# Kernel tuning notes

Hardware: AMD Instinct MI355X
Metric: run time of the kernel (lower is better)

Reference implementation:

```python
import jax, jax.numpy as jnp
import numpy as np

D_MODEL, D_STATE, D_CONV, EXPAND = 1024, 16, 4, 2
D_INNER = EXPAND * D_MODEL
BATCH, SEQ = 2, 2048


def setup_inputs() -> dict:
    key = jax.random.key(0)
    ks = jax.random.split(key, 10)
    s = lambda fan_in: 1.0 / np.sqrt(fan_in)
    return {
        "x": jax.random.normal(ks[0], (BATCH, SEQ, D_MODEL), jnp.float32),
        "W_in": jax.random.normal(ks[1], (2 * D_INNER, D_MODEL), jnp.float32) * s(D_MODEL),
        "w_conv": jax.random.normal(ks[2], (D_INNER, D_CONV), jnp.float32) * s(D_CONV),
        "b_conv": jax.random.normal(ks[3], (D_INNER,), jnp.float32) * 0.02,
        "W_x": jax.random.normal(ks[4], (D_INNER + 2 * D_STATE, D_INNER), jnp.float32) * s(D_INNER),
        "W_dt": jax.random.normal(ks[5], (D_INNER, D_INNER), jnp.float32) * s(D_INNER),
        "b_dt": jax.random.normal(ks[6], (D_INNER,), jnp.float32) * 0.02,
        "A_log": jnp.log(jax.random.uniform(ks[7], (D_INNER, D_STATE), jnp.float32, 1e-4, 1.0)),
        "D": jnp.ones((D_INNER,), jnp.float32),
        "W_out": jax.random.normal(ks[8], (D_MODEL, D_INNER), jnp.float32) * s(D_INNER),
    }


def _depthwise_causal_conv(x, w, b):
    # x: (B, L, C), w: (C, K), causal (left-pad K-1), matches conv1d(padding=K-1)[..., :L]
    K = w.shape[1]
    L = x.shape[1]
    xp = jnp.pad(x, ((0, 0), (K - 1, 0), (0, 0)))
    out = b
    for k in range(K):  # K is tiny (4)
        out = out + xp[:, k:k + L, :] * w[:, k]
    return out


def _selective_scan(x, delta, Bm, Cm, A, Dv):
    # x, delta: (B, L, d_inner); Bm, Cm: (B, L, d_state)
    def step(state, inp):
        x_t, d_t, B_t, C_t = inp  # (B,d_inner),(B,d_inner),(B,d_state),(B,d_state)
        decay = jnp.exp(d_t[..., None] * A)          # (B, d_inner, d_state)
        state = decay * state + B_t[:, None, :] * x_t[..., None]
        y_t = jnp.einsum('bds,bs->bd', state, C_t) + x_t * Dv
        return state, y_t

    init = jnp.zeros((x.shape[0], x.shape[2], A.shape[1]), x.dtype)
    xs = tuple(jnp.swapaxes(a, 0, 1) for a in (x, delta, Bm, Cm))
    _, ys = jax.lax.scan(step, init, xs)             # ys: (L, B, d_inner)
    return jnp.swapaxes(ys, 0, 1)


def reference(x, W_in, w_conv, b_conv, W_x, W_dt, b_dt, A_log, D, W_out):
    silu = jax.nn.silu
    xz = x @ W_in.T                                   # (B, L, 2*d_inner)
    x_inner, z = jnp.split(xz, 2, axis=-1)
    x_conv = silu(_depthwise_causal_conv(x_inner, w_conv, b_conv))
    x_dbl = x_conv @ W_x.T                            # (B, L, d_inner + 2*d_state)
    delta, Bm, Cm = jnp.split(x_dbl, [D_INNER, D_INNER + D_STATE], axis=-1)
    delta = jax.nn.softplus(delta @ W_dt.T + b_dt)
    A = -jnp.exp(A_log.astype(jnp.float32))
    y = _selective_scan(x_conv, delta, Bm, Cm, A, D)
    y = y * silu(z)
    return y @ W_out.T
```

## Files before the change

kernel.cpp:

```cpp
#include <hip/hip_runtime.h>
#include <hip/hip_bf16.h>


#define BATCH 2
#define SEQ   2048
#define DM    1024
#define DI    2048
#define DS    16
#define T_TOK (BATCH * SEQ)

#define CL 64
#define NC 32

typedef __bf16 v8bf __attribute__((ext_vector_type(8)));
typedef float  v4f  __attribute__((ext_vector_type(4)));

__device__ __forceinline__ void gld16(const void* g, void* l) {
    __builtin_amdgcn_global_load_lds(
        (const __attribute__((address_space(1))) void*)g,
        (__attribute__((address_space(3))) void*)l, 16, 0, 0);
}

__device__ __forceinline__ float b2f(__hip_bfloat16 v) { return __bfloat162float(v); }

__global__ void detect_dtype(const unsigned* __restrict__ Dptr, int* __restrict__ flag) {
    if (threadIdx.x == 0 && blockIdx.x == 0)
        *flag = (Dptr[0] == 0x3F803F80u) ? 1 : 0;
}

__device__ __forceinline__ float load_in(const void* p, size_t i, int isbf) {
    return isbf ? b2f(((const __hip_bfloat16*)p)[i]) : ((const float*)p)[i];
}

#define NBIG0 (T_TOK * DM)
#define NBIG1 (4096 * DM)
#define NBIG2 (DI * DI)
#define NBIG3 (DM * DI)
__global__ void convert_big(const void* __restrict__ s0, const void* __restrict__ s1,
                            const void* __restrict__ s2, const void* __restrict__ s3,
                            __hip_bfloat16* __restrict__ d0, __hip_bfloat16* __restrict__ d1,
                            __hip_bfloat16* __restrict__ d2, __hip_bfloat16* __restrict__ d3,
                            const int* __restrict__ flag) {
    if (*flag) return;
    size_t e = ((size_t)blockIdx.x * 256 + threadIdx.x) * 8;
    const float* src; __hip_bfloat16* dst;
    if (e < NBIG0)                      { src = (const float*)s0 + e;                 dst = d0 + e; }
    else if (e < NBIG0 + NBIG1)         { e -= NBIG0; src = (const float*)s1 + e;     dst = d1 + e; }
    else if (e < NBIG0 + NBIG1 + NBIG2) { e -= NBIG0 + NBIG1; src = (const float*)s2 + e; dst = d2 + e; }
    else                                { e -= NBIG0 + NBIG1 + NBIG2; src = (const float*)s3 + e; dst = d3 + e; }
    const float4 a = *(const float4*)src;
    const float4 b = *(const float4*)(src + 4);
    __bf16 o[8] = {(__bf16)a.x,(__bf16)a.y,(__bf16)a.z,(__bf16)a.w,
                   (__bf16)b.x,(__bf16)b.y,(__bf16)b.z,(__bf16)b.w};
    *(uint4*)dst = *(uint4*)&o[0];
}

__global__ void convert_small(const void* __restrict__ wconv, const void* __restrict__ bconv,
                              const void* __restrict__ bdt, const void* __restrict__ dv,
                              __hip_bfloat16* __restrict__ wconvb, __hip_bfloat16* __restrict__ bconvb,
                              __hip_bfloat16* __restrict__ bdtb, __hip_bfloat16* __restrict__ db,
                              const int* __restrict__ flag) {
    const int isbf = *flag;
    const int i = blockIdx.x * 256 + threadIdx.x;
    if (i < 8192)        wconvb[i]        = __float2bfloat16(load_in(wconv, i, isbf));
    else if (i < 10240)  bconvb[i - 8192] = __float2bfloat16(load_in(bconv, i - 8192, isbf));
    else if (i < 12288)  bdtb[i - 10240]  = __float2bfloat16(load_in(bdt, i - 10240, isbf));
    else if (i < 14336)  db[i - 12288]    = __float2bfloat16(load_in(dv, i - 12288, isbf));
}

template <int MODE, int TN>
__global__ __launch_bounds__(256) void gemm_bt(
    const __hip_bfloat16* __restrict__ Ac, const void* __restrict__ Araw,
    const __hip_bfloat16* __restrict__ Bc, const void* __restrict__ Braw,
    void* __restrict__ out0, void* __restrict__ out1,
    const __hip_bfloat16* __restrict__ bias,
    const int* __restrict__ flag,
    int M, int N, int K)
{
    constexpr int NF = TN / 32;
    constexpr int ASLOT = 512;
    constexpr int BSLOT = TN * 4;
    __shared__ v8bf Asv[2 * ASLOT];
    __shared__ v8bf Bsv[2 * BSLOT];

    const int isbf = *flag;
    const __hip_bfloat16* A  = (isbf && Araw) ? (const __hip_bfloat16*)Araw : Ac;
    const __hip_bfloat16* Bw = (isbf && Braw) ? (const __hip_bfloat16*)Braw : Bc;

    const int nx = gridDim.x;
    const int nblk = nx * gridDim.y;
    const int id = blockIdx.y * nx + blockIdx.x;
    const int sid = (id & 7) * (nblk >> 3) + (id >> 3);
    const int bxs = sid % nx;
    const int bys = sid / nx;

    const int tid  = threadIdx.x;
    const int bm   = bys * 128;
    const int bn   = bxs * TN;
    const int w    = tid >> 6;
    const int lane = tid & 63;
    const int wm   = (w >> 1) * 64;
    const int wn   = (w & 1) * (TN / 2);
    const int lrow  = lane & 15;
    const int lquad = lane >> 4;

    v4f acc[4][NF];
#pragma unroll
    for (int i = 0; i < 4; i++)
#pragma unroll
        for (int j = 0; j < NF; j++) acc[i][j] = (v4f){0.f, 0.f, 0.f, 0.f};

    const int r0 = tid >> 2;
    const int q0 = (tid & 3) ^ ((r0 >> 1) & 3);
    const __hip_bfloat16* gA0 = A  + (size_t)(bm + r0) * K + q0 * 8;
    const __hip_bfloat16* gA1 = A  + (size_t)(bm + 64 + r0) * K + q0 * 8;
    const __hip_bfloat16* gB0 = Bw + (size_t)(bn + r0) * K + q0 * 8;
    const __hip_bfloat16* gB1 = Bw + (size_t)(bn + 64 + r0) * K + q0 * 8;
    char* lA0 = (char*)Asv + tid * 16;
    char* lA1 = (char*)Asv + 4096 + tid * 16;
    char* lB0 = (char*)Bsv + tid * 16;
    char* lB1 = (char*)Bsv + 4096 + tid * 16;

    const int swz = lquad ^ ((lrow >> 1) & 3);
    int sA[4], sB[NF];
#pragma unroll
    for (int i = 0; i < 4; i++) sA[i] = (wm + i * 16 + lrow) * 4 + swz;
#pragma unroll
    for (int i = 0; i < NF; i++) sB[i] = (wn + i * 16 + lrow) * 4 + swz;

    const int NIT = K >> 5;
    gld16(gA0, lA0);
    gld16(gA1, lA1);
    gld16(gB0, lB0);
    if (TN == 128) gld16(gB1, lB1);

    int k = 32;
    for (int it = 0; it < NIT; ++it) {
        const int cb = it & 1;
        __syncthreads();
        if (it + 1 < NIT) {
            const int pa = (cb ^ 1) * 8192;
            const int pb = (cb ^ 1) * (BSLOT * 16);
            gld16(gA0 + k, lA0 + pa);
            gld16(gA1 + k, lA1 + pa);
            gld16(gB0 + k, lB0 + pb);
            if (TN == 128) gld16(gB1 + k, lB1 + pb);
            k += 32;
        }
        const int ca = cb * ASLOT;
        const int cbb = cb * BSLOT;
        v8bf af[4], bfr[NF];
#pragma unroll
        for (int i = 0; i < 4; i++)
            af[i] = Asv[ca + sA[i]];
#pragma unroll
        for (int i = 0; i < NF; i++)
            bfr[i] = Bsv[cbb + sB[i]];
#pragma unroll
        for (int mi = 0; mi < 4; mi++)
#pragma unroll
            for (int ni = 0; ni < NF; ni++)
                acc[mi][ni] = __builtin_amdgcn_mfma_f32_16x16x32_bf16(
                    af[mi], bfr[ni], acc[mi][ni], 0, 0, 0);
    }

#pragma unroll
    for (int mi = 0; mi < 4; mi++) {
#pragma unroll
        for (int ni = 0; ni < NF; ni++) {
#pragma unroll
            for (int r = 0; r < 4; r++) {
                const int grow = bm + wm + mi * 16 + lquad * 4 + r;
                const int gcol = bn + wn + ni * 16 + lrow;
                const float v = acc[mi][ni][r];
                if (MODE == 0) {
                    ((__hip_bfloat16*)out0)[(size_t)grow * N + gcol] = __float2bfloat16(v);
                } else if (MODE == 1) {
                    if (gcol < 2048) {
                        ((__hip_bfloat16*)out0)[(size_t)grow * 2048 + gcol] = __float2bfloat16(v);
                    } else if (gcol < 2080) {
                        ((float*)out1)[(size_t)grow * 32 + (gcol - 2048)] = v;
                    }
                } else if (MODE == 2) {
                    const float x = v + b2f(bias[gcol]);
                    const float sp = (x > 15.f) ? x : __logf(1.f + __expf(x));
                    ((__hip_bfloat16*)out0)[(size_t)grow * 2048 + gcol] = __float2bfloat16(sp);
                } else {
                    if (isbf)
                        ((__hip_bfloat16*)out0)[(size_t)grow * N + gcol] = __float2bfloat16(v);
                    else
                        ((float*)out0)[(size_t)grow * N + gcol] = v;
                }
            }
        }
    }
}

__global__ void prep_A(const void* __restrict__ A_log, float* __restrict__ Amat,
                       const int* __restrict__ flag) {
    const int isbf = *flag;
    const int i = blockIdx.x * 256 + threadIdx.x;
    if (i < DI * DS) Amat[i] = -__expf(load_in(A_log, i, isbf));
}

__global__ void pad_Wx(const void* __restrict__ Wx, __hip_bfloat16* __restrict__ Wxp,
                       const int* __restrict__ flag) {
    const int isbf = *flag;
    const size_t e = ((size_t)blockIdx.x * 256 + threadIdx.x) * 8;
    if (e >= (size_t)2176 * 2048) return;
    if (e >= (size_t)2080 * 2048) {
        __bf16 z[8] = {};
        *(uint4*)(Wxp + e) = *(uint4*)&z[0];
        return;
    }
    if (isbf) {
        *(uint4*)(Wxp + e) = *(const uint4*)((const __hip_bfloat16*)Wx + e);
    } else {
        const float* src = (const float*)Wx + e;
        const float4 a = *(const float4*)src;
        const float4 b = *(const float4*)(src + 4);
        __bf16 o[8] = {(__bf16)a.x,(__bf16)a.y,(__bf16)a.z,(__bf16)a.w,
                       (__bf16)b.x,(__bf16)b.y,(__bf16)b.z,(__bf16)b.w};
        *(uint4*)(Wxp + e) = *(uint4*)&o[0];
    }
}

__global__ __launch_bounds__(256) void conv_silu(
    const __hip_bfloat16* __restrict__ xz,
    const __hip_bfloat16* __restrict__ wconv,
    const __hip_bfloat16* __restrict__ bconv,
    __hip_bfloat16* __restrict__ xconv)
{
    const int idx = blockIdx.x * 256 + threadIdx.x;
    const int c8 = (idx & 255) << 3;
    const int tg = idx >> 8;
    const int tl = tg & (SEQ - 1);

    __bf16 wl[32], bl[8];
    *(uint4*)&wl[0]  = *(const uint4*)(wconv + c8 * 4);
    *(uint4*)&wl[8]  = *(const uint4*)(wconv + c8 * 4 + 8);
    *(uint4*)&wl[16] = *(const uint4*)(wconv + c8 * 4 + 16);
    *(uint4*)&wl[24] = *(const uint4*)(wconv + c8 * 4 + 24);
    *(uint4*)&bl[0]  = *(const uint4*)(bconv + c8);

    float acc[8];
#pragma unroll
    for (int cc = 0; cc < 8; cc++) acc[cc] = (float)bl[cc];

#pragma unroll
    for (int k = 0; k < 4; k++) {
        const int ts = tl - 3 + k;
        if (ts >= 0) {
            __bf16 xl[8];
            *(uint4*)&xl[0] = *(const uint4*)(xz + (size_t)(tg - 3 + k) * 4096 + c8);
#pragma unroll
            for (int cc = 0; cc < 8; cc++)
                acc[cc] += (float)wl[cc * 4 + k] * (float)xl[cc];
        }
    }

    __bf16 o[8];
#pragma unroll
    for (int cc = 0; cc < 8; cc++) {
        const float s = acc[cc] / (1.f + __expf(-acc[cc]));
        o[cc] = (__bf16)s;
    }
    *(uint4*)(xconv + (size_t)tg * DI + c8) = *(uint4*)&o[0];
}

__global__ __launch_bounds__(256) void scan_p1(
    const __hip_bfloat16* __restrict__ delta, const __hip_bfloat16* __restrict__ xconv,
    const float* __restrict__ BC, const float* __restrict__ Amat,
    float* __restrict__ Pws, float* __restrict__ Sws)
{
    const int d = blockIdx.x * 256 + threadIdx.x;
    const int c = blockIdx.y;
    const int b = blockIdx.z;
    const int tg0 = b * SEQ + c * CL;

    __shared__ float bc[CL * 32];
    for (int i = threadIdx.x; i < CL * 32; i += 256) bc[i] = BC[(size_t)tg0 * 32 + i];
    __syncthreads();

    float Areg[DS];
#pragma unroll
    for (int s = 0; s < DS; s++) Areg[s] = Amat[d * DS + s];

    float P[DS], S[DS];
#pragma unroll
    for (int s = 0; s < DS; s++) { P[s] = 1.f; S[s] = 0.f; }

    for (int i = 0; i < CL; i++) {
        const size_t tg = tg0 + i;
        const float dl = b2f(delta[tg * DI + d]);
        const float x  = b2f(xconv[tg * DI + d]);
#pragma unroll
        for (int s = 0; s < DS; s++) {
            const float e = __expf(dl * Areg[s]);
            P[s] *= e;
            S[s] = e * S[s] + bc[i * 32 + s] * x;
        }
    }

    const size_t base = (((size_t)b * NC + c) * DI + d) * DS;
#pragma unroll
    for (int s = 0; s < DS; s += 4) {
        *(float4*)(Pws + base + s) = make_float4(P[s], P[s+1], P[s+2], P[s+3]);
        *(float4*)(Sws + base + s) = make_float4(S[s], S[s+1], S[s+2], S[s+3]);
    }
}

__global__ void scan_p2(float* __restrict__ Pws, float* __restrict__ Sws) {
    const int idx = blockIdx.x * 256 + threadIdx.x;
    const int b  = idx >> 15;
    const int ds = idx & 32767;
    float carry = 0.f;
    for (int c = 0; c < NC; c++) {
        const size_t a = (((size_t)b * NC + c) << 15) + ds;
        const float p  = Pws[a];
        const float sv = Sws[a];
        Sws[a] = carry;
        carry = p * carry + sv;
    }
}

__global__ __launch_bounds__(256) void scan_p3(
    const __hip_bfloat16* __restrict__ delta, const __hip_bfloat16* __restrict__ xconv,
    const float* __restrict__ BC, const float* __restrict__ Amat,
    const float* __restrict__ Sws, const __hip_bfloat16* __restrict__ xz,
    const __hip_bfloat16* __restrict__ Dv, __hip_bfloat16* __restrict__ yg)
{
    const int d = blockIdx.x * 256 + threadIdx.x;
    const int c = blockIdx.y;
    const int b = blockIdx.z;
    const int tg0 = b * SEQ + c * CL;

    __shared__ float bc[CL * 32];
    for (int i = threadIdx.x; i < CL * 32; i += 256) bc[i] = BC[(size_t)tg0 * 32 + i];
    __syncthreads();

    float Areg[DS];
#pragma unroll
    for (int s = 0; s < DS; s++) Areg[s] = Amat[d * DS + s];

    const size_t base = (((size_t)b * NC + c) * DI + d) * DS;
    float S[DS];
#pragma unroll
    for (int s = 0; s < DS; s += 4) {
        const float4 v = *(const float4*)(Sws + base + s);
        S[s] = v.x; S[s+1] = v.y; S[s+2] = v.z; S[s+3] = v.w;
    }
    const float Dd = b2f(Dv[d]);

    for (int i = 0; i < CL; i++) {
        const size_t tg = tg0 + i;
        const float dl = b2f(delta[tg * DI + d]);
        const float x  = b2f(xconv[tg * DI + d]);
        float y = 0.f;
#pragma unroll
        for (int s = 0; s < DS; s++) {
            const float e = __expf(dl * Areg[s]);
            S[s] = e * S[s] + bc[i * 32 + s] * x;
            y += S[s] * bc[i * 32 + 16 + s];
        }
        y += x * Dd;
        const float z = b2f(xz[tg * 4096 + 2048 + d]);
        const float g = z / (1.f + __expf(-z));
        yg[tg * DI + d] = __float2bfloat16(y * g);
    }
}

extern "C" void kernel_launch(void* const* d_in, const int* in_sizes, int n_in,
                              void* d_out, int out_size, void* d_ws, size_t ws_size,
                              hipStream_t stream)
{
    const void* x_raw     = d_in[0];
    const void* W_in_raw  = d_in[1];
    const void* wconv_raw = d_in[2];
    const void* bconv_raw = d_in[3];
    const void* W_x_raw   = d_in[4];
    const void* W_dt_raw  = d_in[5];
    const void* b_dt_raw  = d_in[6];
    const void* A_log_raw = d_in[7];
    const void* D_raw     = d_in[8];
    const void* W_out_raw = d_in[9];

    char* ws = (char*)d_ws;
    size_t off = 0;
    auto alloc = [&](size_t bytes) { char* p = ws + off; off += (bytes + 255) & ~(size_t)255; return p; };
    int*            FLAG  = (int*)alloc(256);
    __hip_bfloat16* XB    = (__hip_bfloat16*)alloc((size_t)T_TOK * DM * 2);
    __hip_bfloat16* WINB  = (__hip_bfloat16*)alloc((size_t)4096 * DM * 2);
    __hip_bfloat16* WDTB  = (__hip_bfloat16*)alloc((size_t)DI * DI * 2);
    __hip_bfloat16* WOUTB = (__hip_bfloat16*)alloc((size_t)DM * DI * 2);
    __hip_bfloat16* WCONVB= (__hip_bfloat16*)alloc((size_t)DI * 4 * 2);
    __hip_bfloat16* BCONVB= (__hip_bfloat16*)alloc((size_t)DI * 2);
    __hip_bfloat16* BDTB  = (__hip_bfloat16*)alloc((size_t)DI * 2);
    __hip_bfloat16* DB    = (__hip_bfloat16*)alloc((size_t)DI * 2);
    __hip_bfloat16* XZ    = (__hip_bfloat16*)alloc((size_t)T_TOK * 4096 * 2);
    __hip_bfloat16* XCONV = (__hip_bfloat16*)alloc((size_t)T_TOK * DI * 2);
    __hip_bfloat16* DRAW  = (__hip_bfloat16*)alloc((size_t)T_TOK * DI * 2);
    __hip_bfloat16* WXPAD = (__hip_bfloat16*)alloc((size_t)2176 * DI * 2);
    float*          BC    = (float*)alloc((size_t)T_TOK * 32 * 4);
    __hip_bfloat16* DELTA = (__hip_bfloat16*)alloc((size_t)T_TOK * DI * 2);
    float*          AMAT  = (float*)alloc((size_t)DI * DS * 4);
    float*          PWS   = (float*)alloc((size_t)BATCH * NC * DI * DS * 4);
    float*          SWS   = (float*)alloc((size_t)BATCH * NC * DI * DS * 4);
    __hip_bfloat16* YG    = (__hip_bfloat16*)alloc((size_t)T_TOK * DI * 2);

    detect_dtype<<<1, 64, 0, stream>>>((const unsigned*)D_raw, FLAG);
    convert_big<<<(NBIG0 + NBIG1 + NBIG2 + NBIG3) / (256 * 8), 256, 0, stream>>>(
        x_raw, W_in_raw, W_dt_raw, W_out_raw, XB, WINB, WDTB, WOUTB, FLAG);
    convert_small<<<56, 256, 0, stream>>>(wconv_raw, bconv_raw, b_dt_raw, D_raw,
                                          WCONVB, BCONVB, BDTB, DB, FLAG);
    prep_A<<<(DI * DS + 255) / 256, 256, 0, stream>>>(A_log_raw, AMAT, FLAG);
    pad_Wx<<<(int)(((size_t)2176 * 2048 / 8 + 255) / 256), 256, 0, stream>>>(W_x_raw, WXPAD, FLAG);

    gemm_bt<0, 128><<<dim3(32, 32), 256, 0, stream>>>(
        XB, x_raw, WINB, W_in_raw, XZ, nullptr, nullptr, FLAG, T_TOK, 4096, DM);

    conv_silu<<<T_TOK, 256, 0, stream>>>(XZ, WCONVB, BCONVB, XCONV);

    gemm_bt<1, 128><<<dim3(17, 32), 256, 0, stream>>>(
        XCONV, nullptr, WXPAD, nullptr, DRAW, BC, nullptr, FLAG, T_TOK, 2176, DI);

    gemm_bt<2, 128><<<dim3(16, 32), 256, 0, stream>>>(
        DRAW, nullptr, WDTB, W_dt_raw, DELTA, nullptr, BDTB, FLAG, T_TOK, DI, DI);

    scan_p1<<<dim3(DI / 256, NC, BATCH), 256, 0, stream>>>(DELTA, XCONV, BC, AMAT, PWS, SWS);
    scan_p2<<<(BATCH * DI * DS) / 256, 256, 0, stream>>>(PWS, SWS);
    scan_p3<<<dim3(DI / 256, NC, BATCH), 256, 0, stream>>>(DELTA, XCONV, BC, AMAT, SWS, XZ, DB, YG);

    gemm_bt<3, 64><<<dim3(16, 32), 256, 0, stream>>>(
        YG, nullptr, WOUTB, W_out_raw, d_out, nullptr, nullptr, FLAG, T_TOK, DM, DI);
}
```

Baseline: 464.1 us.

## Add 256x256-tile 8-wave GEMM with 4-stage LDS pipeline for three projections

Adds a new bf16 MFMA GEMM kernel with 256x256 output tiles, 512 threads (8 waves), a 4-buffer global-to-LDS prefetch pipeline with explicit vmcnt waits, swizzled LDS layout, and block-id remapping across groups of eight. It replaces the older 128-wide-tile GEMM for the in-projection, x-projection and dt-projection. W_x padding grows from 2176 to 2304 rows so that N divides evenly by 256, which adds some wasted compute on zero rows. The aim is higher data reuse per tile and better overlap of loads with MFMA work. The cost is a large register footprint and fewer blocks per GPU.

```diff
diff --git a/kernel.cpp b/kernel.cpp
--- a/kernel.cpp
+++ b/kernel.cpp
@@ -66,6 +66,133 @@
     else if (i < 10240)  bconvb[i - 8192] = __float2bfloat16(load_in(bconv, i - 8192, isbf));
     else if (i < 12288)  bdtb[i - 10240]  = __float2bfloat16(load_in(bdt, i - 10240, isbf));
     else if (i < 14336)  db[i - 12288]    = __float2bfloat16(load_in(dv, i - 12288, isbf));
+}
+
+template <int MODE, int KDIM>
+__global__ __launch_bounds__(512, 2) void gemm8p(
+    const __hip_bfloat16* __restrict__ Ac, const void* __restrict__ Araw,
+    const __hip_bfloat16* __restrict__ Bc, const void* __restrict__ Braw,
+    void* __restrict__ out0, void* __restrict__ out1,
+    const __hip_bfloat16* __restrict__ bias,
+    const int* __restrict__ flag,
+    int N)
+{
+    constexpr int NT = KDIM >> 5;
+    __shared__ v8bf lds[8192];
+
+    const int isbf = *flag;
+    const __hip_bfloat16* A  = (isbf && Araw) ? (const __hip_bfloat16*)Araw : Ac;
+    const __hip_bfloat16* Bw = (isbf && Braw) ? (const __hip_bfloat16*)Braw : Bc;
+
+    const int nx = gridDim.x;
+    const int nblk = nx * gridDim.y;
+    const int id = blockIdx.y * nx + blockIdx.x;
+    const int sid = (id & 7) * (nblk >> 3) + (id >> 3);
+    const int bm = (sid / nx) * 256;
+    const int bn = (sid % nx) * 256;
+
+    const int tid   = threadIdx.x;
+    const int lane  = tid & 63;
+    const int w     = tid >> 6;
+    const int wr    = (w >> 2) * 128;
+    const int wc    = (w & 3) * 64;
+    const int lrow  = lane & 15;
+    const int lquad = lane >> 4;
+    const int swz   = lquad ^ ((lrow >> 1) & 3);
+
+    v4f acc[8][4];
+#pragma unroll
+    for (int i = 0; i < 8; i++)
+#pragma unroll
+        for (int j = 0; j < 4; j++) acc[i][j] = (v4f){0.f, 0.f, 0.f, 0.f};
+
+    const int r0 = tid >> 2;
+    const int q0 = (tid & 3) ^ ((r0 >> 1) & 3);
+    const __hip_bfloat16* gA0 = A  + (size_t)(bm + r0) * KDIM + q0 * 8;
+    const __hip_bfloat16* gA1 = gA0 + (size_t)128 * KDIM;
+    const __hip_bfloat16* gB0 = Bw + (size_t)(bn + r0) * KDIM + q0 * 8;
+    const __hip_bfloat16* gB1 = gB0 + (size_t)128 * KDIM;
+    char* lbase = (char*)&lds[0] + tid * 16;
+
+    int sA[8], sB[4];
+#pragma unroll
+    for (int i = 0; i < 8; i++) sA[i] = (wr + i * 16 + lrow) * 4 + swz;
+#pragma unroll
+    for (int i = 0; i < 4; i++) sB[i] = 1024 + (wc + i * 16 + lrow) * 4 + swz;
+
+#define STAGE8(kt, b) do {                         \
+        const size_t ko_ = (size_t)(kt) * 32;      \
+        char* d_ = lbase + (b) * 32768;            \
+        gld16(gA0 + ko_, d_);                      \
+        gld16(gA1 + ko_, d_ + 8192);               \
+        gld16(gB0 + ko_, d_ + 16384);              \
+        gld16(gB1 + ko_, d_ + 24576);              \
+    } while (0)
+
+    STAGE8(0, 0);
+    STAGE8(1, 1);
+    STAGE8(2, 2);
+
+#pragma unroll 4
+    for (int t = 0; t < NT; ++t) {
+        const int cb = t & 3;
+        if (t + 3 < NT) {
+            STAGE8(t + 3, (t + 3) & 3);
+            asm volatile("s_waitcnt vmcnt(12)" ::: "memory");
+        } else if (t + 3 == NT) {
+            asm volatile("s_waitcnt vmcnt(8)" ::: "memory");
+        } else if (t + 2 == NT) {
+            asm volatile("s_waitcnt vmcnt(4)" ::: "memory");
+        } else {
+            asm volatile("s_waitcnt vmcnt(0)" ::: "memory");
+        }
+        __builtin_amdgcn_s_barrier();
+
+        const v8bf* buf = &lds[0] + cb * 2048;
+        v8bf af[8], bfr[4];
+#pragma unroll
+        for (int i = 0; i < 8; i++) af[i] = buf[sA[i]];
+#pragma unroll
+        for (int i = 0; i < 4; i++) bfr[i] = buf[sB[i]];
+        asm volatile("s_waitcnt lgkmcnt(0)" ::: "memory");
+        __builtin_amdgcn_s_barrier();
+
+        __builtin_amdgcn_s_setprio(1);
+#pragma unroll
+        for (int mi = 0; mi < 8; mi++)
+#pragma unroll
+            for (int ni = 0; ni < 4; ni++)
+                acc[mi][ni] = __builtin_amdgcn_mfma_f32_16x16x32_bf16(
+                    af[mi], bfr[ni], acc[mi][ni], 0, 0, 0);
+        __builtin_amdgcn_s_setprio(0);
+    }
+#undef STAGE8
+
+#pragma unroll
+    for (int mi = 0; mi < 8; mi++) {
+#pragma unroll
+        for (int ni = 0; ni < 4; ni++) {
+#pragma unroll
+            for (int r = 0; r < 4; r++) {
+                const int grow = bm + wr + mi * 16 + lquad * 4 + r;
+                const int gcol = bn + wc + ni * 16 + lrow;
+                const float v = acc[mi][ni][r];
+                if (MODE == 0) {
+                    ((__hip_bfloat16*)out0)[(size_t)grow * N + gcol] = __float2bfloat16(v);
+                } else if (MODE == 1) {
+                    if (gcol < 2048) {
+                        ((__hip_bfloat16*)out0)[(size_t)grow * 2048 + gcol] = __float2bfloat16(v);
+                    } else if (gcol < 2080) {
+                        ((float*)out1)[(size_t)grow * 32 + (gcol - 2048)] = v;
+                    }
+                } else {
+                    const float x = v + b2f(bias[gcol]);
+                    const float sp = (x > 15.f) ? x : __logf(1.f + __expf(x));
+                    ((__hip_bfloat16*)out0)[(size_t)grow * 2048 + gcol] = __float2bfloat16(sp);
+                }
+            }
+        }
+    }
 }
 
 template <int MODE, int TN>
@@ -207,7 +334,7 @@
                        const int* __restrict__ flag) {
     const int isbf = *flag;
     const size_t e = ((size_t)blockIdx.x * 256 + threadIdx.x) * 8;
-    if (e >= (size_t)2176 * 2048) return;
+    if (e >= (size_t)2304 * 2048) return;
     if (e >= (size_t)2080 * 2048) {
         __bf16 z[8] = {};
         *(uint4*)(Wxp + e) = *(uint4*)&z[0];
@@ -400,7 +527,7 @@
     __hip_bfloat16* XZ    = (__hip_bfloat16*)alloc((size_t)T_TOK * 4096 * 2);
     __hip_bfloat16* XCONV = (__hip_bfloat16*)alloc((size_t)T_TOK * DI * 2);
     __hip_bfloat16* DRAW  = (__hip_bfloat16*)alloc((size_t)T_TOK * DI * 2);
-    __hip_bfloat16* WXPAD = (__hip_bfloat16*)alloc((size_t)2176 * DI * 2);
+    __hip_bfloat16* WXPAD = (__hip_bfloat16*)alloc((size_t)2304 * DI * 2);
     float*          BC    = (float*)alloc((size_t)T_TOK * 32 * 4);
     __hip_bfloat16* DELTA = (__hip_bfloat16*)alloc((size_t)T_TOK * DI * 2);
     float*          AMAT  = (float*)alloc((size_t)DI * DS * 4);
@@ -414,18 +541,18 @@
     convert_small<<<56, 256, 0, stream>>>(wconv_raw, bconv_raw, b_dt_raw, D_raw,
                                           WCONVB, BCONVB, BDTB, DB, FLAG);
     prep_A<<<(DI * DS + 255) / 256, 256, 0, stream>>>(A_log_raw, AMAT, FLAG);
-    pad_Wx<<<(int)(((size_t)2176 * 2048 / 8 + 255) / 256), 256, 0, stream>>>(W_x_raw, WXPAD, FLAG);
-
-    gemm_bt<0, 128><<<dim3(32, 32), 256, 0, stream>>>(
-        XB, x_raw, WINB, W_in_raw, XZ, nullptr, nullptr, FLAG, T_TOK, 4096, DM);
+    pad_Wx<<<(int)(((size_t)2304 * 2048 / 8 + 255) / 256), 256, 0, stream>>>(W_x_raw, WXPAD, FLAG);
+
+    gemm8p<0, 1024><<<dim3(16, 16), 512, 0, stream>>>(
+        XB, x_raw, WINB, W_in_raw, XZ, nullptr, nullptr, FLAG, 4096);
 
     conv_silu<<<T_TOK, 256, 0, stream>>>(XZ, WCONVB, BCONVB, XCONV);
 
-    gemm_bt<1, 128><<<dim3(17, 32), 256, 0, stream>>>(
-        XCONV, nullptr, WXPAD, nullptr, DRAW, BC, nullptr, FLAG, T_TOK, 2176, DI);
-
-    gemm_bt<2, 128><<<dim3(16, 32), 256, 0, stream>>>(
-        DRAW, nullptr, WDTB, W_dt_raw, DELTA, nullptr, BDTB, FLAG, T_TOK, DI, DI);
+    gemm8p<1, 2048><<<dim3(9, 16), 512, 0, stream>>>(
+        XCONV, nullptr, WXPAD, nullptr, DRAW, BC, nullptr, FLAG, 2304);
+
+    gemm8p<2, 2048><<<dim3(8, 16), 512, 0, stream>>>(
+        DRAW, nullptr, WDTB, W_dt_raw, DELTA, nullptr, BDTB, FLAG, 2048);
 
     scan_p1<<<dim3(DI / 256, NC, BATCH), 256, 0, stream>>>(DELTA, XCONV, BC, AMAT, PWS, SWS);
     scan_p2<<<(BATCH * DI * DS) / 256, 256, 0, stream>>>(PWS, SWS);
```

New measurement: 468.7 us. About the same (+1.0%).

## Fold W_dt into W_x weights to fuse delta projection GEMMs

Applied to the files above, without the earlier changes.

Precomputes the product of W_dt and the delta rows of W_x as a weight-only GEMM (after transposing W_x), so the per-token delta projection becomes a single GEMM with fused bias+softplus alongside the B/C outputs. This removes one token-sized GEMM and the intermediate DRAW buffer round trip. It also merges the A_log prep into convert_small. The cost is an extra transpose and a 2048^3 weight GEMM per call, and a change in rounding since the combined weight is rounded to bf16.

```diff
diff --git a/kernel.cpp b/kernel.cpp
--- a/kernel.cpp
+++ b/kernel.cpp
@@ -57,8 +57,10 @@
 
 __global__ void convert_small(const void* __restrict__ wconv, const void* __restrict__ bconv,
                               const void* __restrict__ bdt, const void* __restrict__ dv,
+                              const void* __restrict__ A_log,
                               __hip_bfloat16* __restrict__ wconvb, __hip_bfloat16* __restrict__ bconvb,
                               __hip_bfloat16* __restrict__ bdtb, __hip_bfloat16* __restrict__ db,
+                              float* __restrict__ Amat,
                               const int* __restrict__ flag) {
     const int isbf = *flag;
     const int i = blockIdx.x * 256 + threadIdx.x;
@@ -66,6 +68,68 @@
     else if (i < 10240)  bconvb[i - 8192] = __float2bfloat16(load_in(bconv, i - 8192, isbf));
     else if (i < 12288)  bdtb[i - 10240]  = __float2bfloat16(load_in(bdt, i - 10240, isbf));
     else if (i < 14336)  db[i - 12288]    = __float2bfloat16(load_in(dv, i - 12288, isbf));
+    else if (i < 47104)  Amat[i - 14336]  = -__expf(load_in(A_log, i - 14336, isbf));
+}
+
+__global__ __launch_bounds__(256) void transpose_wxd(
+    const void* __restrict__ Wx, __hip_bfloat16* __restrict__ WxdT,
+    const int* __restrict__ flag)
+{
+    const int isbf = *flag;
+    __shared__ __bf16 t[64][72];
+    const int bi = blockIdx.y * 64;
+    const int bj = blockIdx.x * 64;
+    const int rr = threadIdx.x >> 3;
+    const int c0 = (threadIdx.x & 7) * 8;
+
+#pragma unroll
+    for (int k = 0; k < 2; k++) {
+        const int r = rr + k * 32;
+        const size_t src = (size_t)(bi + r) * DI + bj + c0;
+        __bf16 o[8];
+        if (isbf) {
+            *(uint4*)&o[0] = *(const uint4*)((const __hip_bfloat16*)Wx + src);
+        } else {
+            const float* s = (const float*)Wx + src;
+            const float4 a = *(const float4*)s;
+            const float4 b = *(const float4*)(s + 4);
+            o[0]=(__bf16)a.x; o[1]=(__bf16)a.y; o[2]=(__bf16)a.z; o[3]=(__bf16)a.w;
+            o[4]=(__bf16)b.x; o[5]=(__bf16)b.y; o[6]=(__bf16)b.z; o[7]=(__bf16)b.w;
+        }
+        *(uint4*)&t[r][c0] = *(uint4*)&o[0];
+    }
+    __syncthreads();
+#pragma unroll
+    for (int k = 0; k < 2; k++) {
+        const int dr = rr + k * 32;
+        __bf16 o[8];
+#pragma unroll
+        for (int j = 0; j < 8; j++) o[j] = t[c0 + j][dr];
+        *(uint4*)(WxdT + (size_t)(bj + dr) * DI + bi + c0) = *(uint4*)&o[0];
+    }
+}
+
+__global__ void pad_bc(const void* __restrict__ Wx, __hip_bfloat16* __restrict__ Wxp,
+                       const int* __restrict__ flag) {
+    const int isbf = *flag;
+    const size_t e = ((size_t)blockIdx.x * 256 + threadIdx.x) * 8;
+    if (e >= (size_t)128 * DI) return;
+    const size_t base = (size_t)2048 * DI;
+    if (e >= (size_t)32 * DI) {
+        __bf16 z[8] = {};
+        *(uint4*)(Wxp + base + e) = *(uint4*)&z[0];
+        return;
+    }
+    if (isbf) {
+        *(uint4*)(Wxp + base + e) = *(const uint4*)((const __hip_bfloat16*)Wx + base + e);
+    } else {
+        const float* src = (const float*)Wx + base + e;
+        const float4 a = *(const float4*)src;
+        const float4 b = *(const float4*)(src + 4);
+        __bf16 o[8] = {(__bf16)a.x,(__bf16)a.y,(__bf16)a.z,(__bf16)a.w,
+                       (__bf16)b.x,(__bf16)b.y,(__bf16)b.z,(__bf16)b.w};
+        *(uint4*)(Wxp + base + e) = *(uint4*)&o[0];
+    }
 }
 
 template <int MODE, int TN>
@@ -175,16 +239,14 @@
                 const float v = acc[mi][ni][r];
                 if (MODE == 0) {
                     ((__hip_bfloat16*)out0)[(size_t)grow * N + gcol] = __float2bfloat16(v);
-                } else if (MODE == 1) {
+                } else if (MODE == 4) {
                     if (gcol < 2048) {
-                        ((__hip_bfloat16*)out0)[(size_t)grow * 2048 + gcol] = __float2bfloat16(v);
+                        const float x = v + b2f(bias[gcol]);
+                        const float sp = (x > 15.f) ? x : __logf(1.f + __expf(x));
+                        ((__hip_bfloat16*)out0)[(size_t)grow * 2048 + gcol] = __float2bfloat16(sp);
                     } else if (gcol < 2080) {
                         ((float*)out1)[(size_t)grow * 32 + (gcol - 2048)] = v;
                     }
-                } else if (MODE == 2) {
-                    const float x = v + b2f(bias[gcol]);
-                    const float sp = (x > 15.f) ? x : __logf(1.f + __expf(x));
-                    ((__hip_bfloat16*)out0)[(size_t)grow * 2048 + gcol] = __float2bfloat16(sp);
                 } else {
                     if (isbf)
                         ((__hip_bfloat16*)out0)[(size_t)grow * N + gcol] = __float2bfloat16(v);
@@ -193,35 +255,6 @@
                 }
             }
         }
-    }
-}
-
-__global__ void prep_A(const void* __restrict__ A_log, float* __restrict__ Amat,
-                       const int* __restrict__ flag) {
-    const int isbf = *flag;
-    const int i = blockIdx.x * 256 + threadIdx.x;
-    if (i < DI * DS) Amat[i] = -__expf(load_in(A_log, i, isbf));
-}
-
-__global__ void pad_Wx(const void* __restrict__ Wx, __hip_bfloat16* __restrict__ Wxp,
-                       const int* __restrict__ flag) {
-    const int isbf = *flag;
-    const size_t e = ((size_t)blockIdx.x * 256 + threadIdx.x) * 8;
-    if (e >= (size_t)2176 * 2048) return;
-    if (e >= (size_t)2080 * 2048) {
-        __bf16 z[8] = {};
-        *(uint4*)(Wxp + e) = *(uint4*)&z[0];
-        return;
-    }
-    if (isbf) {
-        *(uint4*)(Wxp + e) = *(const uint4*)((const __hip_bfloat16*)Wx + e);
-    } else {
-        const float* src = (const float*)Wx + e;
-        const float4 a = *(const float4*)src;
-        const float4 b = *(const float4*)(src + 4);
-        __bf16 o[8] = {(__bf16)a.x,(__bf16)a.y,(__bf16)a.z,(__bf16)a.w,
-                       (__bf16)b.x,(__bf16)b.y,(__bf16)b.z,(__bf16)b.w};
-        *(uint4*)(Wxp + e) = *(uint4*)&o[0];
     }
 }
 
@@ -399,7 +432,7 @@
     __hip_bfloat16* DB    = (__hip_bfloat16*)alloc((size_t)DI * 2);
     __hip_bfloat16* XZ    = (__hip_bfloat16*)alloc((size_t)T_TOK * 4096 * 2);
     __hip_bfloat16* XCONV = (__hip_bfloat16*)alloc((size_t)T_TOK * DI * 2);
-    __hip_bfloat16* DRAW  = (__hip_bfloat16*)alloc((size_t)T_TOK * DI * 2);
+    __hip_bfloat16* WXDT  = (__hip_bfloat16*)alloc((size_t)DI * DI * 2);
     __hip_bfloat16* WXPAD = (__hip_bfloat16*)alloc((size_t)2176 * DI * 2);
     float*          BC    = (float*)alloc((size_t)T_TOK * 32 * 4);
     __hip_bfloat16* DELTA = (__hip_bfloat16*)alloc((size_t)T_TOK * DI * 2);
@@ -411,21 +444,22 @@
     detect_dtype<<<1, 64, 0, stream>>>((const unsigned*)D_raw, FLAG);
     convert_big<<<(NBIG0 + NBIG1 + NBIG2 + NBIG3) / (256 * 8), 256, 0, stream>>>(
         x_raw, W_in_raw, W_dt_raw, W_out_raw, XB, WINB, WDTB, WOUTB, FLAG);
-    convert_small<<<56, 256, 0, stream>>>(wconv_raw, bconv_raw, b_dt_raw, D_raw,
-                                          WCONVB, BCONVB, BDTB, DB, FLAG);
-    prep_A<<<(DI * DS + 255) / 256, 256, 0, stream>>>(A_log_raw, AMAT, FLAG);
-    pad_Wx<<<(int)(((size_t)2176 * 2048 / 8 + 255) / 256), 256, 0, stream>>>(W_x_raw, WXPAD, FLAG);
+    convert_small<<<184, 256, 0, stream>>>(wconv_raw, bconv_raw, b_dt_raw, D_raw, A_log_raw,
+                                           WCONVB, BCONVB, BDTB, DB, AMAT, FLAG);
+    transpose_wxd<<<dim3(32, 32), 256, 0, stream>>>(W_x_raw, WXDT, FLAG);
+
+    gemm_bt<0, 128><<<dim3(16, 16), 256, 0, stream>>>(
+        WDTB, W_dt_raw, WXDT, nullptr, WXPAD, nullptr, nullptr, FLAG, DI, DI, DI);
+
+    pad_bc<<<128, 256, 0, stream>>>(W_x_raw, WXPAD, FLAG);
 
     gemm_bt<0, 128><<<dim3(32, 32), 256, 0, stream>>>(
         XB, x_raw, WINB, W_in_raw, XZ, nullptr, nullptr, FLAG, T_TOK, 4096, DM);
 
     conv_silu<<<T_TOK, 256, 0, stream>>>(XZ, WCONVB, BCONVB, XCONV);
 
-    gemm_bt<1, 128><<<dim3(17, 32), 256, 0, stream>>>(
-        XCONV, nullptr, WXPAD, nullptr, DRAW, BC, nullptr, FLAG, T_TOK, 2176, DI);
-
-    gemm_bt<2, 128><<<dim3(16, 32), 256, 0, stream>>>(
-        DRAW, nullptr, WDTB, W_dt_raw, DELTA, nullptr, BDTB, FLAG, T_TOK, DI, DI);
+    gemm_bt<4, 128><<<dim3(17, 32), 256, 0, stream>>>(
+        XCONV, nullptr, WXPAD, nullptr, DELTA, BC, BDTB, FLAG, T_TOK, 2176, DI);
 
     scan_p1<<<dim3(DI / 256, NC, BATCH), 256, 0, stream>>>(DELTA, XCONV, BC, AMAT, PWS, SWS);
     scan_p2<<<(BATCH * DI * DS) / 256, 256, 0, stream>>>(PWS, SWS);
```

New measurement: 468.6 us. No clear change (+1.0%).
